# Performance work log

Measured on AMD Instinct MI355X. Metric: run time of the kernel, lower is better.

## Reference

```python
import jax, jax.numpy as jnp
import numpy as np

L, H, C, DH, FF = 6, 8, 512, 64, 2048
B, T, S = 64, 128, 128
EPS = 1e-5


def setup_inputs() -> dict:
    key = jax.random.key(0)
    ks = jax.random.split(key, 20)
    sc = 0.02
    def w(k, shape):
        return jax.random.normal(k, shape, dtype=jnp.float32) * sc
    inp = {
        "x": jax.random.normal(ks[0], (B, T, C), dtype=jnp.float32),
        "encoder_output": jax.random.normal(ks[1], (B, S, C), dtype=jnp.float32),
        # per-head self-attention projections, stacked over layers and heads
        "sa_wq": w(ks[2], (L, H, C, DH)), "sa_bq": w(ks[3], (L, H, DH)),
        "sa_wk": w(ks[4], (L, H, C, DH)), "sa_bk": w(ks[5], (L, H, DH)),
        "sa_wv": w(ks[6], (L, H, C, DH)), "sa_bv": w(ks[7], (L, H, DH)),
        # per-head cross-attention projections
        "ca_wq": w(ks[8], (L, H, C, DH)), "ca_bq": w(ks[9], (L, H, DH)),
        "ca_wk": w(ks[10], (L, H, C, DH)), "ca_bk": w(ks[11], (L, H, DH)),
        "ca_wv": w(ks[12], (L, H, C, DH)), "ca_bv": w(ks[13], (L, H, DH)),
        # feed-forward
        "ff_w1": w(ks[14], (L, C, FF)), "ff_b1": w(ks[15], (L, FF)),
        "ff_w2": w(ks[16], (L, FF, C)), "ff_b2": w(ks[17], (L, C)),
    }
    return inp


def _layer_norm_2d(x):
    # F.layer_norm(x, (T, C)): normalize jointly over last two dims, no affine
    mu = jnp.mean(x, axis=(1, 2), keepdims=True)
    var = jnp.var(x, axis=(1, 2), keepdims=True)
    return (x - mu) * jax.lax.rsqrt(var + EPS)


def _mha(qx, kvx, wq, bq, wk, bk, wv, bv):
    # wq/wk/wv: [H, C, DH]; per-head projections, vectorized over heads.
    q = jnp.einsum("btc,hcd->bhtd", qx, wq) + bq[:, None, :]
    k = jnp.einsum("bsc,hcd->bhsd", kvx, wk) + bk[:, None, :]
    v = jnp.einsum("bsc,hcd->bhsd", kvx, wv) + bv[:, None, :]
    scores = jax.nn.softmax(jnp.einsum("bhtd,bhsd->bhts", q, k) * (DH ** -0.5), axis=-1)
    out = jnp.einsum("bhts,bhsd->bhtd", scores, v)
    b, h, t, d = out.shape  # concat heads along feature dim
    return out.transpose(0, 2, 1, 3).reshape(b, t, h * d)


def reference(x, encoder_output, sa_wq, sa_bq, sa_wk, sa_bk, sa_wv, sa_bv,
              ca_wq, ca_bq, ca_wk, ca_bk, ca_wv, ca_bv,
              ff_w1, ff_b1, ff_w2, ff_b2):
    for l in range(L):
        # masked MHA (note: original code never applies the causal mask)
        x = x + _mha(x, x, sa_wq[l], sa_bq[l], sa_wk[l], sa_bk[l], sa_wv[l], sa_bv[l])
        x = _layer_norm_2d(x)
        # cross attention: q from decoder, k/v from encoder output
        x = x + _mha(x, encoder_output, ca_wq[l], ca_bq[l], ca_wk[l], ca_bk[l], ca_wv[l], ca_bv[l])
        x = _layer_norm_2d(x)
        # feed-forward
        h = jax.nn.relu(jnp.einsum("btc,cf->btf", x, ff_w1[l]) + ff_b1[l])
        x = x + (jnp.einsum("btf,fc->btc", h, ff_w2[l]) + ff_b2[l])
        x = _layer_norm_2d(x)
    return x
```

## Files before the change

kernel.cpp:

```cpp
#include <hip/hip_runtime.h>
#include <hip/hip_bf16.h>


typedef __bf16 bf16;
typedef bf16 bf16x8 __attribute__((ext_vector_type(8)));
typedef float f32x4 __attribute__((ext_vector_type(4)));

#define MFMA16(a, b, c) __builtin_amdgcn_mfma_f32_16x16x32_bf16(a, b, c, 0, 0, 0)

#define GLL16(gsrc, ldst)                                                          \
    __builtin_amdgcn_global_load_lds(                                              \
        (const __attribute__((address_space(1))) void*)(gsrc),                     \
        (__attribute__((address_space(3))) void*)(ldst), 16, 0, 0)

static constexpr int L_ = 6, C_ = 512, FF_ = 2048;
static constexpr int B_ = 64, T_ = 128;
static constexpr int M_ = B_ * T_;
static constexpr float LNINV = 1.f / 65536.f;
static constexpr float EPS_ = 1e-5f;

__global__ __launch_bounds__(256) void zero_all(
    float* __restrict__ csA, float* __restrict__ csQ, float* __restrict__ csF,
    float* __restrict__ part)
{
    const int i = blockIdx.x * 256 + threadIdx.x;
    if (i < 6 * 1536) csA[i] = 0.f;
    if (i < 6 * 512)  csQ[i] = 0.f;
    if (i < 6 * 2048) csF[i] = 0.f;
    if (i < 18 * 64 * 2) part[i] = 0.f;
}

__global__ __launch_bounds__(256) void init_x(
    const float* __restrict__ xin, float* __restrict__ y, bf16* __restrict__ yb)
{
    const size_t i = ((size_t)blockIdx.x * 256 + threadIdx.x) * 8;
    float4 f0 = *(const float4*)(xin + i);
    float4 f1 = *(const float4*)(xin + i + 4);
    *(float4*)(y + i) = f0;
    *(float4*)(y + i + 4) = f1;
    bf16x8 v = {(bf16)f0.x, (bf16)f0.y, (bf16)f0.z, (bf16)f0.w,
                (bf16)f1.x, (bf16)f1.y, (bf16)f1.z, (bf16)f1.w};
    *(bf16x8*)(yb + i) = v;
}

__global__ __launch_bounds__(256) void to_bf16(
    const float* __restrict__ in, bf16* __restrict__ out)
{
    const size_t i = ((size_t)blockIdx.x * 256 + threadIdx.x) * 8;
    float4 f0 = *(const float4*)(in + i);
    float4 f1 = *(const float4*)(in + i + 4);
    bf16x8 v = {(bf16)f0.x, (bf16)f0.y, (bf16)f0.z, (bf16)f0.w,
                (bf16)f1.x, (bf16)f1.y, (bf16)f1.z, (bf16)f1.w};
    *(bf16x8*)(out + i) = v;
}

__global__ __launch_bounds__(256) void transpose_f32_bf16(
    const float* __restrict__ src, bf16* __restrict__ dst, int R, int C)
{
    __shared__ alignas(16) float t[64][68];
    const int r0 = blockIdx.y * 64, c0 = blockIdx.x * 64;
    const int tr = threadIdx.x >> 4;
    const int tc = (threadIdx.x & 15) * 4;
#pragma unroll
    for (int ro = 0; ro < 64; ro += 16)
        *(float4*)&t[tr + ro][tc] = *(const float4*)(src + (size_t)(r0 + tr + ro) * C + c0 + tc);
    __syncthreads();
    const int wc = (threadIdx.x & 7) * 8;
#pragma unroll
    for (int po = 0; po < 2; ++po) {
        const int oc = (threadIdx.x >> 3) + po * 32;
        bf16x8 v;
#pragma unroll
        for (int j = 0; j < 8; ++j) v[j] = (bf16)t[wc + j][oc];
        *(bf16x8*)(dst + (size_t)(c0 + oc) * R + r0 + wc) = v;
    }
}

__global__ __launch_bounds__(256) void head_repack(
    const float* __restrict__ sa_wq, const float* __restrict__ sa_wk,
    const float* __restrict__ sa_wv, const float* __restrict__ ca_wq,
    const float* __restrict__ ca_wk, const float* __restrict__ ca_wv,
    bf16* __restrict__ Wsa, bf16* __restrict__ Wcaq, bf16* __restrict__ Wcakv)
{
    __shared__ alignas(16) float t[64][68];
    const int z = blockIdx.z;
    const int type = z / 48, rem = z % 48, l = rem >> 3, h = rem & 7;
    const float* srcs[6] = {sa_wq, sa_wk, sa_wv, ca_wq, ca_wk, ca_wv};
    const float* s = srcs[type] + (size_t)(l * 8 + h) * 512 * 64;
    bf16* d;
    if (type < 3)       d = Wsa   + ((size_t)l * 1536 + type * 512 + h * 64) * 512;
    else if (type == 3) d = Wcaq  + ((size_t)l * 512 + h * 64) * 512;
    else                d = Wcakv + ((size_t)l * 1024 + (type - 4) * 512 + h * 64) * 512;
    const int r0 = blockIdx.y * 64;
    const int tr = threadIdx.x >> 4;
    const int tc = (threadIdx.x & 15) * 4;
#pragma unroll
    for (int ro = 0; ro < 64; ro += 16)
        *(float4*)&t[tr + ro][tc] = *(const float4*)(s + (size_t)(r0 + tr + ro) * 64 + tc);
    __syncthreads();
    const int wc = (threadIdx.x & 7) * 8;
#pragma unroll
    for (int po = 0; po < 2; ++po) {
        const int oc = (threadIdx.x >> 3) + po * 32;
        bf16x8 v;
#pragma unroll
        for (int j = 0; j < 8; ++j) v[j] = (bf16)t[wc + j][oc];
        *(bf16x8*)(d + (size_t)oc * 512 + r0 + wc) = v;
    }
}

__global__ __launch_bounds__(256) void colsum_all(
    const float* __restrict__ sa_wq, const float* __restrict__ sa_wk,
    const float* __restrict__ sa_wv, const float* __restrict__ ca_wq,
    const float* __restrict__ ff_w1,
    float* __restrict__ csA, float* __restrict__ csQ, float* __restrict__ csF)
{
    const int t = blockIdx.x * 256 + threadIdx.x;
    const int l = t >> 12, u = t & 4095;
    const int r0 = blockIdx.y * 64;
    const float* base;
    int stride;
    float* out;
    if (u < 1536) {
        const int p = u >> 9, h = (u >> 6) & 7, d = u & 63;
        const float* w = (p == 0) ? sa_wq : (p == 1) ? sa_wk : sa_wv;
        base = w + (size_t)(l * 8 + h) * 512 * 64 + d;
        stride = 64;
        out = &csA[l * 1536 + u];
    } else if (u < 2048) {
        const int v = u - 1536, h = v >> 6, d = v & 63;
        base = ca_wq + (size_t)(l * 8 + h) * 512 * 64 + d;
        stride = 64;
        out = &csQ[l * 512 + v];
    } else {
        const int f = u - 2048;
        base = ff_w1 + (size_t)l * 512 * 2048 + f;
        stride = 2048;
        out = &csF[l * 2048 + f];
    }
    const float* p = base + (size_t)r0 * stride;
    float s0 = 0.f, s1 = 0.f, s2 = 0.f, s3 = 0.f;
#pragma unroll 4
    for (int c = 0; c < 64; c += 4) {
        s0 += p[0];
        s1 += p[(size_t)stride];
        s2 += p[(size_t)2 * stride];
        s3 += p[(size_t)3 * stride];
        p += (size_t)4 * stride;
    }
    atomicAdd(out, (s0 + s1) + (s2 + s3));
}

template <int MODE, int BM>
__global__ __launch_bounds__(512) void gemm_bt(
    const bf16* __restrict__ A, const bf16* __restrict__ BT,
    const float* __restrict__ b0, const float* __restrict__ b1,
    const float* __restrict__ b2, const float* __restrict__ cs,
    float2* __restrict__ part, int slotPrev, int slotNew,
    bf16* __restrict__ o0, bf16* __restrict__ o1, bf16* __restrict__ o2,
    float* __restrict__ y, bf16* __restrict__ ybf, int N, int K)
{
    constexpr int WC = (BM == 256) ? 2 : 4;
    constexpr int MI = 4;
    constexpr int NI = (BM == 256) ? 4 : 2;
    constexpr int AR = BM / 8;
    constexpr int AGLL = BM / 64;
    constexpr int VG = AGLL + 2;
    __shared__ alignas(16) bf16 as[2][BM][64];
    __shared__ alignas(16) bf16 bs[2][128][64];
    const int tid = threadIdx.x, wave = tid >> 6, lane = tid & 63;

    const int gx = gridDim.x;
    int wgid = blockIdx.y * gx + blockIdx.x;
    {
        const int nwg = gx * gridDim.y;
        const int q = nwg >> 3, r = nwg & 7;
        const int xcd = wgid & 7, idx = wgid >> 3;
        wgid = (xcd < r ? xcd * (q + 1) : r * (q + 1) + (xcd - r) * q) + idx;
    }
    const int m0 = (wgid / gx) * BM, n0 = (wgid % gx) * 128;

    const int wr = ((WC == 2) ? (wave >> 1) : (wave >> 2)) * 64;
    const int wc = (wave & (WC - 1)) * (128 / WC);
    const int fr = lane & 15, fq = lane >> 4;
    const int xr = fr & 7;

    float mu = 0.f, rstd = 1.f;
    if (slotPrev >= 0) {
        float2 p = part[slotPrev * 64 + ((m0 + wr) >> 7)];
        mu = p.x * LNINV;
        rstd = rsqrtf(p.y * LNINV - mu * mu + EPS_);
    }

    const int rlane = lane >> 3;
    const int scol = ((lane & 7) ^ rlane) * 8;
    const bf16* pa = A + (size_t)(m0 + wave * AR + rlane) * K + scol;
    const bf16* pb = BT + (size_t)(n0 + wave * 16 + rlane) * K + scol;

    auto stage = [&](int buf, int k0) {
#pragma unroll
        for (int i = 0; i < AGLL; ++i)
            GLL16(pa + k0 + (size_t)(8 * i) * K, &as[buf][wave * AR + 8 * i][0]);
#pragma unroll
        for (int i = 0; i < 2; ++i)
            GLL16(pb + k0 + (size_t)(8 * i) * K, &bs[buf][wave * 16 + 8 * i][0]);
    };

    f32x4 acc[MI][NI] = {};
    bf16x8 af[MI], bfv[NI];
    auto frags = [&](int buf, int kk) {
#pragma unroll
        for (int mi = 0; mi < MI; ++mi)
            af[mi] = *(const bf16x8*)&as[buf][wr + mi * 16 + fr][(((kk << 2) + fq) ^ xr) << 3];
#pragma unroll
        for (int ni = 0; ni < NI; ++ni)
            bfv[ni] = *(const bf16x8*)&bs[buf][wc + ni * 16 + fr][(((kk << 2) + fq) ^ xr) << 3];
    };
    auto cluster = [&]() {
        __builtin_amdgcn_s_setprio(1);
#pragma unroll
        for (int mi = 0; mi < MI; ++mi)
#pragma unroll
            for (int ni = 0; ni < NI; ++ni)
                acc[mi][ni] = MFMA16(af[mi], bfv[ni], acc[mi][ni]);
        __builtin_amdgcn_s_setprio(0);
    };

    const int nt = K >> 6;
    stage(0, 0);
    stage(1, 64);

    int cur = 0;
    for (int t = 0; t < nt - 1; ++t) {
        asm volatile("s_waitcnt vmcnt(%0)\n\ts_barrier" :: "n"(VG) : "memory");
        frags(cur, 0);
        asm volatile("s_waitcnt lgkmcnt(0)" ::: "memory");
        __builtin_amdgcn_sched_barrier(0);
        cluster();
        frags(cur, 1);
        asm volatile("s_waitcnt lgkmcnt(0)" ::: "memory");
        __builtin_amdgcn_sched_barrier(0);
        __builtin_amdgcn_s_barrier();
        if (t + 2 < nt) stage(cur, (t + 2) << 6);
        cluster();
        cur ^= 1;
    }
    asm volatile("s_waitcnt vmcnt(0)\n\ts_barrier" ::: "memory");
    frags(cur, 0);
    asm volatile("s_waitcnt lgkmcnt(0)" ::: "memory");
    __builtin_amdgcn_sched_barrier(0);
    cluster();
    frags(cur, 1);
    asm volatile("s_waitcnt lgkmcnt(0)" ::: "memory");
    __builtin_amdgcn_sched_barrier(0);
    cluster();

    float s = 0.f, ss = 0.f;
    const float murs = mu * rstd;
#pragma unroll
    for (int mi = 0; mi < MI; ++mi) {
#pragma unroll
        for (int ni = 0; ni < NI; ++ni) {
            const int n = n0 + wc + ni * 16 + fr;
#pragma unroll
            for (int reg = 0; reg < 4; ++reg) {
                const int r = m0 + wr + mi * 16 + fq * 4 + reg;
                float val = acc[mi][ni][reg];
                if constexpr (MODE == 0) {
                    const int p = n >> 9, hd = n & 511, d = n & 63, hh = (n >> 6) & 7;
                    const int bb = r >> 7, tt = r & 127;
                    const float* bias = (p == 0) ? b0 : (p == 1 ? b1 : b2);
                    val = val * rstd + bias[hd] - murs * cs[n];
                    const size_t bh = (size_t)(bb * 8 + hh);
                    if (p == 0)      o0[(bh * 128 + tt) * 64 + d] = (bf16)val;
                    else if (p == 1) o1[(bh * 128 + tt) * 64 + d] = (bf16)val;
                    else             o2[(bh * 64 + d) * 128 + tt] = (bf16)val;
                } else if constexpr (MODE == 1) {
                    const int d = n & 63, hh = (n >> 6) & 7;
                    const int bb = r >> 7, tt = r & 127;
                    val = val * rstd + b0[n] - murs * cs[n];
                    o0[((size_t)(bb * 8 + hh) * 128 + tt) * 64 + d] = (bf16)val;
                } else if constexpr (MODE == 2) {
                    const int p = n >> 9, hd = n & 511, d = n & 63, hh = (n >> 6) & 7;
                    const int bb = r >> 7, tt = r & 127;
                    val += (p == 0) ? b1[hd] : b2[hd];
                    const size_t bh = (size_t)(bb * 8 + hh);
                    if (p == 0) o1[(bh * 128 + tt) * 64 + d] = (bf16)val;
                    else        o2[(bh * 64 + d) * 128 + tt] = (bf16)val;
                } else if constexpr (MODE == 3) {
                    val = val * rstd + b0[n] - murs * cs[n];
                    val = fmaxf(val, 0.f);
                    o0[(size_t)r * 2048 + n] = (bf16)val;
                } else {
                    const size_t idx = (size_t)r * 512 + n;
                    const float v = (y[idx] - mu) * rstd + val + b0[n];
                    y[idx] = v;
                    ybf[idx] = (bf16)v;
                    s += v;
                    ss += v * v;
                }
            }
        }
    }
    if constexpr (MODE == 4) {
        for (int off = 32; off; off >>= 1) { s += __shfl_xor(s, off); ss += __shfl_xor(ss, off); }
        __shared__ float rs[8], rss[8];
        if (lane == 0) { rs[wave] = s; rss[wave] = ss; }
        __syncthreads();
        if (tid == 0) {
            float sa = 0.f, sb = 0.f;
#pragma unroll
            for (int w = 0; w < 8; ++w) { sa += rs[w]; sb += rss[w]; }
            float2* dst = &part[slotNew * 64 + (m0 >> 7)];
            atomicAdd(&dst->x, sa);
            atomicAdd(&dst->y, sb);
        }
    }
}

__global__ __launch_bounds__(256) void attn_kernel(
    const bf16* __restrict__ q, const bf16* __restrict__ k,
    const bf16* __restrict__ vT, float* __restrict__ y, bf16* __restrict__ ybf,
    float2* __restrict__ part, int slotPrev, int slotNew)
{
    __shared__ alignas(16) bf16 sP[128][136];
    __shared__ float sPart[2][128];
    const int bh = blockIdx.x;
    const int bb = bh >> 3, hh = bh & 7;
    const bf16* Q = q + (size_t)bh * 128 * 64;
    const bf16* Kp = k + (size_t)bh * 128 * 64;
    const bf16* V = vT + (size_t)bh * 64 * 128;
    const int tid = threadIdx.x, wave = tid >> 6, lane = tid & 63;
    const int wr = (wave >> 1) * 64, wc = (wave & 1) * 64;
    const int fr = lane & 15, fq = lane >> 4;

    float mu = 0.f, rstd = 1.f;
    if (slotPrev >= 0) {
        float2 p = part[slotPrev * 64 + bb];
        mu = p.x * LNINV;
        rstd = rsqrtf(p.y * LNINV - mu * mu + EPS_);
    }

    f32x4 acc[4][4] = {};
#pragma unroll
    for (int k0 = 0; k0 < 64; k0 += 32) {
        bf16x8 af[4], bfv[4];
#pragma unroll
        for (int mi = 0; mi < 4; ++mi)
            af[mi] = *(const bf16x8*)(Q + (size_t)(wr + mi * 16 + fr) * 64 + k0 + fq * 8);
#pragma unroll
        for (int ni = 0; ni < 4; ++ni)
            bfv[ni] = *(const bf16x8*)(Kp + (size_t)(wc + ni * 16 + fr) * 64 + k0 + fq * 8);
#pragma unroll
        for (int mi = 0; mi < 4; ++mi)
#pragma unroll
            for (int ni = 0; ni < 4; ++ni)
                acc[mi][ni] = MFMA16(af[mi], bfv[ni], acc[mi][ni]);
    }

    const int colw = wave & 1;
#pragma unroll
    for (int mi = 0; mi < 4; ++mi) {
#pragma unroll
        for (int reg = 0; reg < 4; ++reg) {
            const int r = wr + mi * 16 + fq * 4 + reg;
            float rsum = 0.f;
#pragma unroll
            for (int ni = 0; ni < 4; ++ni) {
                const float e = __expf(acc[mi][ni][reg] * 0.125f);
                sP[r][wc + ni * 16 + fr] = (bf16)e;
                rsum += e;
            }
            rsum += __shfl_xor(rsum, 1);
            rsum += __shfl_xor(rsum, 2);
            rsum += __shfl_xor(rsum, 4);
            rsum += __shfl_xor(rsum, 8);
            if (fr == 0) sPart[colw][r] = rsum;
        }
    }
    __syncthreads();

    f32x4 acc2[2][4] = {};
#pragma unroll
    for (int k0 = 0; k0 < 128; k0 += 32) {
        bf16x8 af[2], bfv[4];
#pragma unroll
        for (int mi = 0; mi < 2; ++mi)
            af[mi] = *(const bf16x8*)&sP[wave * 32 + mi * 16 + fr][k0 + fq * 8];
#pragma unroll
        for (int ni = 0; ni < 4; ++ni)
            bfv[ni] = *(const bf16x8*)(V + (size_t)(ni * 16 + fr) * 128 + k0 + fq * 8);
#pragma unroll
        for (int mi = 0; mi < 2; ++mi)
#pragma unroll
            for (int ni = 0; ni < 4; ++ni)
                acc2[mi][ni] = MFMA16(af[mi], bfv[ni], acc2[mi][ni]);
    }

    float inv[2][4];
#pragma unroll
    for (int mi = 0; mi < 2; ++mi)
#pragma unroll
        for (int reg = 0; reg < 4; ++reg) {
            const int r = wave * 32 + mi * 16 + fq * 4 + reg;
            inv[mi][reg] = 1.f / (sPart[0][r] + sPart[1][r]);
        }

    float s = 0.f, ss = 0.f;
#pragma unroll
    for (int mi = 0; mi < 2; ++mi)
#pragma unroll
        for (int ni = 0; ni < 4; ++ni)
#pragma unroll
            for (int reg = 0; reg < 4; ++reg) {
                const int r = wave * 32 + mi * 16 + fq * 4 + reg;
                const int d = ni * 16 + fr;
                const size_t idx = ((size_t)(bb * 128 + r)) * 512 + hh * 64 + d;
                const float v = (y[idx] - mu) * rstd + acc2[mi][ni][reg] * inv[mi][reg];
                y[idx] = v;
                ybf[idx] = (bf16)v;
                s += v;
                ss += v * v;
            }
    for (int off = 32; off; off >>= 1) { s += __shfl_xor(s, off); ss += __shfl_xor(ss, off); }
    __shared__ float rs[4], rss[4];
    if (lane == 0) { rs[wave] = s; rss[wave] = ss; }
    __syncthreads();
    if (tid == 0) {
        float2* dst = &part[slotNew * 64 + bb];
        atomicAdd(&dst->x, rs[0] + rs[1] + rs[2] + rs[3]);
        atomicAdd(&dst->y, rss[0] + rss[1] + rss[2] + rss[3]);
    }
}

__global__ __launch_bounds__(256) void final_norm(
    const float* __restrict__ y, const float2* __restrict__ part, int slot,
    float* __restrict__ out)
{
    const size_t i = ((size_t)blockIdx.x * 256 + threadIdx.x) * 4;
    const int b = (int)(i >> 16);
    float2 p = part[slot * 64 + b];
    const float mu = p.x * LNINV;
    const float rstd = rsqrtf(p.y * LNINV - mu * mu + EPS_);
    float4 v = *(const float4*)(y + i);
    float4 o = {(v.x - mu) * rstd, (v.y - mu) * rstd, (v.z - mu) * rstd, (v.w - mu) * rstd};
    *(float4*)(out + i) = o;
}

extern "C" void kernel_launch(void* const* d_in, const int* in_sizes, int n_in,
                              void* d_out, int out_size, void* d_ws, size_t ws_size,
                              hipStream_t stream)
{
    (void)in_sizes; (void)n_in; (void)out_size; (void)ws_size;
    const float* x_in  = (const float*)d_in[0];
    const float* enc   = (const float*)d_in[1];
    const float* sa_wq = (const float*)d_in[2];
    const float* sa_bq = (const float*)d_in[3];
    const float* sa_wk = (const float*)d_in[4];
    const float* sa_bk = (const float*)d_in[5];
    const float* sa_wv = (const float*)d_in[6];
    const float* sa_bv = (const float*)d_in[7];
    const float* ca_wq = (const float*)d_in[8];
    const float* ca_bq = (const float*)d_in[9];
    const float* ca_wk = (const float*)d_in[10];
    const float* ca_bk = (const float*)d_in[11];
    const float* ca_wv = (const float*)d_in[12];
    const float* ca_bv = (const float*)d_in[13];
    const float* ff_w1 = (const float*)d_in[14];
    const float* ff_b1 = (const float*)d_in[15];
    const float* ff_w2 = (const float*)d_in[16];
    const float* ff_b2 = (const float*)d_in[17];

    char* wsp = (char*)d_ws;
    auto alloc = [&](size_t bytes) -> char* {
        char* p = wsp;
        wsp += (bytes + 255) & ~(size_t)255;
        return p;
    };
    float* y     = (float*)alloc((size_t)M_ * 512 * 4);
    bf16*  ybf   = (bf16*)alloc((size_t)M_ * 512 * 2);
    bf16*  encbf = (bf16*)alloc((size_t)M_ * 512 * 2);
    char*  shreg = alloc((size_t)M_ * 2048 * 2);
    bf16*  WsaA  = (bf16*)alloc((size_t)L_ * 1536 * 512 * 2);
    bf16*  WcaqA = (bf16*)alloc((size_t)L_ * 512 * 512 * 2);
    bf16*  WcakvA= (bf16*)alloc((size_t)L_ * 1024 * 512 * 2);
    bf16*  Wff1  = (bf16*)alloc((size_t)2048 * 512 * 2);
    bf16*  Wff2  = (bf16*)alloc((size_t)512 * 2048 * 2);
    float* csA   = (float*)alloc((size_t)L_ * 1536 * 4);
    float* csQ   = (float*)alloc((size_t)L_ * 512 * 4);
    float* csF   = (float*)alloc((size_t)L_ * 2048 * 4);
    float2* part = (float2*)alloc(18 * 64 * sizeof(float2));

    bf16* qb   = (bf16*)shreg;
    bf16* kb   = (bf16*)(shreg + (size_t)512 * 128 * 64 * 2);
    bf16* vTb  = (bf16*)(shreg + (size_t)2 * 512 * 128 * 64 * 2);
    bf16* hbuf = (bf16*)shreg;

    dim3 tb(256), tbg(512);
    zero_all<<<48, tb, 0, stream>>>(csA, csQ, csF, (float*)part);
    init_x<<<2048, tb, 0, stream>>>(x_in, y, ybf);
    to_bf16<<<2048, tb, 0, stream>>>(enc, encbf);
    head_repack<<<dim3(1, 8, 288), tb, 0, stream>>>(sa_wq, sa_wk, sa_wv, ca_wq, ca_wk, ca_wv,
                                                    WsaA, WcaqA, WcakvA);
    colsum_all<<<dim3(96, 8), tb, 0, stream>>>(sa_wq, sa_wk, sa_wv, ca_wq, ff_w1, csA, csQ, csF);

    for (int l = 0; l < L_; ++l) {
        transpose_f32_bf16<<<dim3(32, 8, 1), tb, 0, stream>>>(ff_w1 + (size_t)l * 512 * 2048, Wff1, 512, 2048);
        transpose_f32_bf16<<<dim3(8, 32, 1), tb, 0, stream>>>(ff_w2 + (size_t)l * 2048 * 512, Wff2, 2048, 512);
        const int sPrev = (l == 0) ? -1 : (l - 1) * 3 + 2;
        gemm_bt<0, 256><<<dim3(12, 32), tbg, 0, stream>>>(ybf, WsaA + (size_t)l * 1536 * 512,
            sa_bq + l * 512, sa_bk + l * 512, sa_bv + l * 512, csA + l * 1536,
            part, sPrev, -1, qb, kb, vTb, nullptr, nullptr, 1536, 512);
        attn_kernel<<<512, tb, 0, stream>>>(qb, kb, vTb, y, ybf, part, sPrev, l * 3 + 0);
        gemm_bt<1, 128><<<dim3(4, 64), tbg, 0, stream>>>(ybf, WcaqA + (size_t)l * 512 * 512,
            ca_bq + l * 512, nullptr, nullptr, csQ + l * 512,
            part, l * 3 + 0, -1, qb, nullptr, nullptr, nullptr, nullptr, 512, 512);
        gemm_bt<2, 256><<<dim3(8, 32), tbg, 0, stream>>>(encbf, WcakvA + (size_t)l * 1024 * 512,
            nullptr, ca_bk + l * 512, ca_bv + l * 512, nullptr,
            part, -1, -1, nullptr, kb, vTb, nullptr, nullptr, 1024, 512);
        attn_kernel<<<512, tb, 0, stream>>>(qb, kb, vTb, y, ybf, part, l * 3 + 0, l * 3 + 1);
        gemm_bt<3, 256><<<dim3(16, 32), tbg, 0, stream>>>(ybf, Wff1,
            ff_b1 + l * 2048, nullptr, nullptr, csF + l * 2048,
            part, l * 3 + 1, -1, hbuf, nullptr, nullptr, nullptr, nullptr, 2048, 512);
        gemm_bt<4, 128><<<dim3(4, 64), tbg, 0, stream>>>(hbuf, Wff2,
            ff_b2 + l * 512, nullptr, nullptr, nullptr,
            part, l * 3 + 1, l * 3 + 2, nullptr, nullptr, nullptr, y, ybf, 512, 2048);
    }
    final_norm<<<4096, tb, 0, stream>>>(y, part, 17, (float*)d_out);
}
```

Baseline: 1.400 ms.

## Shrink GEMM tiles to 128xBN with 256 threads and batch FF weight repack

Reworks the GEMM kernel: 256-thread blocks with 128-row M tiles, a BN of 64 or 128, and K steps of 32 instead of 64. Launch bounds now allow four blocks per CU, aiming for more resident blocks and a shorter single-fragment inner loop. It also replaces the twelve per-layer FF weight transposes with one batched ff_repack launch into per-layer buffers. The costs are more workspace memory, more blocks and barriers per unit of K, and smaller tiles with less data reuse.

```diff
diff --git a/kernel.cpp b/kernel.cpp
--- a/kernel.cpp
+++ b/kernel.cpp
@@ -54,11 +54,28 @@
     *(bf16x8*)(out + i) = v;
 }
 
-__global__ __launch_bounds__(256) void transpose_f32_bf16(
-    const float* __restrict__ src, bf16* __restrict__ dst, int R, int C)
+__global__ __launch_bounds__(256) void ff_repack(
+    const float* __restrict__ ff_w1, const float* __restrict__ ff_w2,
+    bf16* __restrict__ W1, bf16* __restrict__ W2)
 {
     __shared__ alignas(16) float t[64][68];
-    const int r0 = blockIdx.y * 64, c0 = blockIdx.x * 64;
+    const int z = blockIdx.z;
+    const float* src;
+    bf16* dst;
+    int R, C, r0, c0;
+    if (z < 6) {
+        src = ff_w1 + (size_t)z * 512 * 2048;
+        dst = W1 + (size_t)z * 2048 * 512;
+        R = 512; C = 2048;
+        r0 = blockIdx.y * 64;
+        c0 = blockIdx.x * 64;
+    } else {
+        src = ff_w2 + (size_t)(z - 6) * 2048 * 512;
+        dst = W2 + (size_t)(z - 6) * 512 * 2048;
+        R = 2048; C = 512;
+        r0 = (blockIdx.y * 4 + (blockIdx.x >> 3)) * 64;
+        c0 = (blockIdx.x & 7) * 64;
+    }
     const int tr = threadIdx.x >> 4;
     const int tc = (threadIdx.x & 15) * 4;
 #pragma unroll
@@ -151,8 +168,8 @@
     atomicAdd(out, (s0 + s1) + (s2 + s3));
 }
 
-template <int MODE, int BM>
-__global__ __launch_bounds__(512) void gemm_bt(
+template <int MODE, int BN>
+__global__ __launch_bounds__(256, 4) void gemm_bt(
     const bf16* __restrict__ A, const bf16* __restrict__ BT,
     const float* __restrict__ b0, const float* __restrict__ b1,
     const float* __restrict__ b2, const float* __restrict__ cs,
@@ -160,14 +177,12 @@
     bf16* __restrict__ o0, bf16* __restrict__ o1, bf16* __restrict__ o2,
     float* __restrict__ y, bf16* __restrict__ ybf, int N, int K)
 {
-    constexpr int WC = (BM == 256) ? 2 : 4;
     constexpr int MI = 4;
-    constexpr int NI = (BM == 256) ? 4 : 2;
-    constexpr int AR = BM / 8;
-    constexpr int AGLL = BM / 64;
-    constexpr int VG = AGLL + 2;
-    __shared__ alignas(16) bf16 as[2][BM][64];
-    __shared__ alignas(16) bf16 bs[2][128][64];
+    constexpr int NI = BN / 32;
+    constexpr int BGLL = BN / 64;
+    constexpr int VG = 2 + BGLL;
+    __shared__ alignas(16) bf16 as[2][128][32];
+    __shared__ alignas(16) bf16 bs[2][BN][32];
     const int tid = threadIdx.x, wave = tid >> 6, lane = tid & 63;
 
     const int gx = gridDim.x;
@@ -178,81 +193,67 @@
         const int xcd = wgid & 7, idx = wgid >> 3;
         wgid = (xcd < r ? xcd * (q + 1) : r * (q + 1) + (xcd - r) * q) + idx;
     }
-    const int m0 = (wgid / gx) * BM, n0 = (wgid % gx) * 128;
-
-    const int wr = ((WC == 2) ? (wave >> 1) : (wave >> 2)) * 64;
-    const int wc = (wave & (WC - 1)) * (128 / WC);
+    const int m0 = (wgid / gx) * 128, n0 = (wgid % gx) * BN;
+
+    const int wr = (wave >> 1) * 64;
+    const int wc = (wave & 1) * (BN / 2);
     const int fr = lane & 15, fq = lane >> 4;
-    const int xr = fr & 7;
+    const int xr = fr & 3;
 
     float mu = 0.f, rstd = 1.f;
     if (slotPrev >= 0) {
-        float2 p = part[slotPrev * 64 + ((m0 + wr) >> 7)];
+        float2 p = part[slotPrev * 64 + (m0 >> 7)];
         mu = p.x * LNINV;
         rstd = rsqrtf(p.y * LNINV - mu * mu + EPS_);
     }
 
-    const int rlane = lane >> 3;
-    const int scol = ((lane & 7) ^ rlane) * 8;
-    const bf16* pa = A + (size_t)(m0 + wave * AR + rlane) * K + scol;
-    const bf16* pb = BT + (size_t)(n0 + wave * 16 + rlane) * K + scol;
+    const int rlane = lane >> 2;
+    const int scol = ((lane & 3) ^ (rlane & 3)) * 8;
+    const bf16* pa = A + (size_t)(m0 + wave * 32 + rlane) * K + scol;
+    const bf16* pb = BT + (size_t)(n0 + wave * (BGLL * 16) + rlane) * K + scol;
 
     auto stage = [&](int buf, int k0) {
 #pragma unroll
-        for (int i = 0; i < AGLL; ++i)
-            GLL16(pa + k0 + (size_t)(8 * i) * K, &as[buf][wave * AR + 8 * i][0]);
-#pragma unroll
         for (int i = 0; i < 2; ++i)
-            GLL16(pb + k0 + (size_t)(8 * i) * K, &bs[buf][wave * 16 + 8 * i][0]);
+            GLL16(pa + k0 + (size_t)(16 * i) * K, &as[buf][wave * 32 + 16 * i][0]);
+#pragma unroll
+        for (int i = 0; i < BGLL; ++i)
+            GLL16(pb + k0 + (size_t)(16 * i) * K, &bs[buf][wave * (BGLL * 16) + 16 * i][0]);
     };
 
     f32x4 acc[MI][NI] = {};
     bf16x8 af[MI], bfv[NI];
-    auto frags = [&](int buf, int kk) {
+    auto frags = [&](int buf) {
 #pragma unroll
         for (int mi = 0; mi < MI; ++mi)
-            af[mi] = *(const bf16x8*)&as[buf][wr + mi * 16 + fr][(((kk << 2) + fq) ^ xr) << 3];
+            af[mi] = *(const bf16x8*)&as[buf][wr + mi * 16 + fr][(fq ^ xr) << 3];
 #pragma unroll
         for (int ni = 0; ni < NI; ++ni)
-            bfv[ni] = *(const bf16x8*)&bs[buf][wc + ni * 16 + fr][(((kk << 2) + fq) ^ xr) << 3];
+            bfv[ni] = *(const bf16x8*)&bs[buf][wc + ni * 16 + fr][(fq ^ xr) << 3];
     };
     auto cluster = [&]() {
-        __builtin_amdgcn_s_setprio(1);
 #pragma unroll
         for (int mi = 0; mi < MI; ++mi)
 #pragma unroll
             for (int ni = 0; ni < NI; ++ni)
                 acc[mi][ni] = MFMA16(af[mi], bfv[ni], acc[mi][ni]);
-        __builtin_amdgcn_s_setprio(0);
     };
 
-    const int nt = K >> 6;
+    const int nt = K >> 5;
     stage(0, 0);
-    stage(1, 64);
+    stage(1, 32);
 
     int cur = 0;
     for (int t = 0; t < nt - 1; ++t) {
         asm volatile("s_waitcnt vmcnt(%0)\n\ts_barrier" :: "n"(VG) : "memory");
-        frags(cur, 0);
-        asm volatile("s_waitcnt lgkmcnt(0)" ::: "memory");
-        __builtin_amdgcn_sched_barrier(0);
-        cluster();
-        frags(cur, 1);
-        asm volatile("s_waitcnt lgkmcnt(0)" ::: "memory");
-        __builtin_amdgcn_sched_barrier(0);
-        __builtin_amdgcn_s_barrier();
-        if (t + 2 < nt) stage(cur, (t + 2) << 6);
+        frags(cur);
+        asm volatile("s_waitcnt lgkmcnt(0)\n\ts_barrier" ::: "memory");
+        if (t + 2 < nt) stage(cur, (t + 2) << 5);
         cluster();
         cur ^= 1;
     }
     asm volatile("s_waitcnt vmcnt(0)\n\ts_barrier" ::: "memory");
-    frags(cur, 0);
-    asm volatile("s_waitcnt lgkmcnt(0)" ::: "memory");
-    __builtin_amdgcn_sched_barrier(0);
-    cluster();
-    frags(cur, 1);
-    asm volatile("s_waitcnt lgkmcnt(0)" ::: "memory");
-    __builtin_amdgcn_sched_barrier(0);
+    frags(cur);
     cluster();
 
     float s = 0.f, ss = 0.f;
@@ -304,16 +305,13 @@
     }
     if constexpr (MODE == 4) {
         for (int off = 32; off; off >>= 1) { s += __shfl_xor(s, off); ss += __shfl_xor(ss, off); }
-        __shared__ float rs[8], rss[8];
+        __shared__ float rs[4], rss[4];
         if (lane == 0) { rs[wave] = s; rss[wave] = ss; }
         __syncthreads();
         if (tid == 0) {
-            float sa = 0.f, sb = 0.f;
-#pragma unroll
-            for (int w = 0; w < 8; ++w) { sa += rs[w]; sb += rss[w]; }
             float2* dst = &part[slotNew * 64 + (m0 >> 7)];
-            atomicAdd(&dst->x, sa);
-            atomicAdd(&dst->y, sb);
+            atomicAdd(&dst->x, rs[0] + rs[1] + rs[2] + rs[3]);
+            atomicAdd(&dst->y, rss[0] + rss[1] + rss[2] + rss[3]);
         }
     }
 }
@@ -484,8 +482,8 @@
     bf16*  WsaA  = (bf16*)alloc((size_t)L_ * 1536 * 512 * 2);
     bf16*  WcaqA = (bf16*)alloc((size_t)L_ * 512 * 512 * 2);
     bf16*  WcakvA= (bf16*)alloc((size_t)L_ * 1024 * 512 * 2);
-    bf16*  Wff1  = (bf16*)alloc((size_t)2048 * 512 * 2);
-    bf16*  Wff2  = (bf16*)alloc((size_t)512 * 2048 * 2);
+    bf16*  Wff1A = (bf16*)alloc((size_t)L_ * 2048 * 512 * 2);
+    bf16*  Wff2A = (bf16*)alloc((size_t)L_ * 512 * 2048 * 2);
     float* csA   = (float*)alloc((size_t)L_ * 1536 * 4);
     float* csQ   = (float*)alloc((size_t)L_ * 512 * 4);
     float* csF   = (float*)alloc((size_t)L_ * 2048 * 4);
@@ -496,33 +494,32 @@
     bf16* vTb  = (bf16*)(shreg + (size_t)2 * 512 * 128 * 64 * 2);
     bf16* hbuf = (bf16*)shreg;
 
-    dim3 tb(256), tbg(512);
+    dim3 tb(256);
     zero_all<<<48, tb, 0, stream>>>(csA, csQ, csF, (float*)part);
     init_x<<<2048, tb, 0, stream>>>(x_in, y, ybf);
     to_bf16<<<2048, tb, 0, stream>>>(enc, encbf);
     head_repack<<<dim3(1, 8, 288), tb, 0, stream>>>(sa_wq, sa_wk, sa_wv, ca_wq, ca_wk, ca_wv,
                                                     WsaA, WcaqA, WcakvA);
+    ff_repack<<<dim3(32, 8, 12), tb, 0, stream>>>(ff_w1, ff_w2, Wff1A, Wff2A);
     colsum_all<<<dim3(96, 8), tb, 0, stream>>>(sa_wq, sa_wk, sa_wv, ca_wq, ff_w1, csA, csQ, csF);
 
     for (int l = 0; l < L_; ++l) {
-        transpose_f32_bf16<<<dim3(32, 8, 1), tb, 0, stream>>>(ff_w1 + (size_t)l * 512 * 2048, Wff1, 512, 2048);
-        transpose_f32_bf16<<<dim3(8, 32, 1), tb, 0, stream>>>(ff_w2 + (size_t)l * 2048 * 512, Wff2, 2048, 512);
         const int sPrev = (l == 0) ? -1 : (l - 1) * 3 + 2;
-        gemm_bt<0, 256><<<dim3(12, 32), tbg, 0, stream>>>(ybf, WsaA + (size_t)l * 1536 * 512,
+        gemm_bt<0, 128><<<dim3(12, 64), tb, 0, stream>>>(ybf, WsaA + (size_t)l * 1536 * 512,
             sa_bq + l * 512, sa_bk + l * 512, sa_bv + l * 512, csA + l * 1536,
             part, sPrev, -1, qb, kb, vTb, nullptr, nullptr, 1536, 512);
         attn_kernel<<<512, tb, 0, stream>>>(qb, kb, vTb, y, ybf, part, sPrev, l * 3 + 0);
-        gemm_bt<1, 128><<<dim3(4, 64), tbg, 0, stream>>>(ybf, WcaqA + (size_t)l * 512 * 512,
+        gemm_bt<1, 64><<<dim3(8, 64), tb, 0, stream>>>(ybf, WcaqA + (size_t)l * 512 * 512,
             ca_bq + l * 512, nullptr, nullptr, csQ + l * 512,
             part, l * 3 + 0, -1, qb, nullptr, nullptr, nullptr, nullptr, 512, 512);
-        gemm_bt<2, 256><<<dim3(8, 32), tbg, 0, stream>>>(encbf, WcakvA + (size_t)l * 1024 * 512,
+        gemm_bt<2, 128><<<dim3(8, 64), tb, 0, stream>>>(encbf, WcakvA + (size_t)l * 1024 * 512,
             nullptr, ca_bk + l * 512, ca_bv + l * 512, nullptr,
             part, -1, -1, nullptr, kb, vTb, nullptr, nullptr, 1024, 512);
         attn_kernel<<<512, tb, 0, stream>>>(qb, kb, vTb, y, ybf, part, l * 3 + 0, l * 3 + 1);
-        gemm_bt<3, 256><<<dim3(16, 32), tbg, 0, stream>>>(ybf, Wff1,
+        gemm_bt<3, 128><<<dim3(16, 64), tb, 0, stream>>>(ybf, Wff1A + (size_t)l * 2048 * 512,
             ff_b1 + l * 2048, nullptr, nullptr, csF + l * 2048,
             part, l * 3 + 1, -1, hbuf, nullptr, nullptr, nullptr, nullptr, 2048, 512);
-        gemm_bt<4, 128><<<dim3(4, 64), tbg, 0, stream>>>(hbuf, Wff2,
+        gemm_bt<4, 64><<<dim3(8, 64), tb, 0, stream>>>(hbuf, Wff2A + (size_t)l * 512 * 2048,
             ff_b2 + l * 512, nullptr, nullptr, nullptr,
             part, l * 3 + 1, l * 3 + 2, nullptr, nullptr, nullptr, y, ybf, 512, 2048);
     }
```

After: 1.320 ms. -5.7%, faster.
